# Performance work log

Measured on AMD Instinct MI355X. Metric: run time of the kernel, lower is better.

The kernel has to match this reference:

```python
import jax, jax.numpy as jnp
import numpy as np
import math

NP_, NA_ = 100000, 50000          # paper / author node counts
E0, E1, E2 = 300000, 300000, 200000  # author->paper, paper->author, paper->paper
H, D = 4, 16
HID = H * D                       # 64
IN_DIM, OUT_DIM = 128, 64
L = 2                             # num_layers
EPS = 1e-5


def _lin(x, W, b):
    return x @ W + b


def _ln(x, g, b):
    m = jnp.mean(x, axis=-1, keepdims=True)
    v = jnp.mean((x - m) ** 2, axis=-1, keepdims=True)
    return (x - m) * jax.lax.rsqrt(v + EPS) * g + b


def _segment_softmax(a, seg, n):
    m = jax.ops.segment_max(a, seg, num_segments=n)
    a = jnp.exp(a - m[seg])
    s = jax.ops.segment_sum(a, seg, num_segments=n)
    return a / (s[seg] + 1e-16)


def _hgt_conv(h_p, h_a, ei_ap, ei_pa, ei_pp,
              W_kqv, b_kqv, W_krel, W_vrel, p_rel, W_hout, b_hout, skip):
    # per-node-type fused KQV projection (HeteroDictLinear)
    kqv_p = _lin(h_p, W_kqv[0], b_kqv[0])   # [NP, 3*HID]
    kqv_a = _lin(h_a, W_kqv[1], b_kqv[1])   # [NA, 3*HID]
    k_p, q_p, v_p = [t.reshape(-1, H, D) for t in jnp.split(kqv_p, 3, axis=1)]
    k_a, q_a, v_a = [t.reshape(-1, H, D) for t in jnp.split(kqv_a, 3, axis=1)]
    # destination (query) concat order: paper then author -> dst offsets {paper:0, author:NP}
    Q = jnp.concatenate([q_p, q_a], axis=0)                    # [NP+NA, H, D]
    # per-(edge_type, head) DxD relation transforms on source k/v (k_rel / v_rel)
    # src concat order follows edge types: et0 src=author, et1 src=paper, et2 src=paper
    Ks = jnp.concatenate([
        jnp.einsum('nhd,hde->nhe', k_a, W_krel[0]),
        jnp.einsum('nhd,hde->nhe', k_p, W_krel[1]),
        jnp.einsum('nhd,hde->nhe', k_p, W_krel[2]),
    ], axis=0)                                                 # [NA+2*NP, H, D]
    Vs = jnp.concatenate([
        jnp.einsum('nhd,hde->nhe', v_a, W_vrel[0]),
        jnp.einsum('nhd,hde->nhe', v_p, W_vrel[1]),
        jnp.einsum('nhd,hde->nhe', v_p, W_vrel[2]),
    ], axis=0)
    # bipartite global edge index (src offsets: 0, NA, NA+NP; dst offsets: paper 0, author NP)
    src = jnp.concatenate([ei_ap[0], ei_pa[0] + NA_, ei_pp[0] + NA_ + NP_])
    dst = jnp.concatenate([ei_ap[1], ei_pa[1] + NP_, ei_pp[1]])
    p = jnp.concatenate([
        jnp.broadcast_to(p_rel[0], (E0, H)),
        jnp.broadcast_to(p_rel[1], (E1, H)),
        jnp.broadcast_to(p_rel[2], (E2, H)),
    ], axis=0)                                                 # [E, H]
    # edge-wise attention: alpha = (q_i * k_j).sum(-1) * p_rel / sqrt(D), segment-softmax over dst
    alpha = jnp.einsum('ehd,ehd->eh', Q[dst], Ks[src]) * p / math.sqrt(D)
    alpha = _segment_softmax(alpha, dst, NP_ + NA_)
    out = jax.ops.segment_sum(Vs[src] * alpha[:, :, None], dst,
                              num_segments=NP_ + NA_)          # [NP+NA, H, D]
    out = out.reshape(-1, HID)
    g = jax.nn.gelu(out, approximate=False)
    o_p = _lin(g[:NP_], W_hout[0], b_hout[0])
    o_a = _lin(g[NP_:], W_hout[1], b_hout[1])
    a_p = jax.nn.sigmoid(skip[0])
    a_a = jax.nn.sigmoid(skip[1])
    return a_p * o_p + (1.0 - a_p) * h_p, a_a * o_a + (1.0 - a_a) * h_a


def _forward(x_paper, x_author, ei_ap, ei_pa, ei_pp,
             W_in, b_in, W_kqv, b_kqv, W_krel, W_vrel, p_rel,
             W_hout, b_hout, skip, ln_g, ln_b, W_out, b_out):
    h_p = _lin(x_paper, W_in[0], b_in[0])
    h_a = _lin(x_author, W_in[1], b_in[1])
    for l in range(L):
        h_p, h_a = _hgt_conv(h_p, h_a, ei_ap, ei_pa, ei_pp,
                             W_kqv[l], b_kqv[l], W_krel[l], W_vrel[l],
                             p_rel[l], W_hout[l], b_hout[l], skip[l])
        h_p = jax.nn.gelu(_ln(h_p, ln_g[l, 0], ln_b[l, 0]), approximate=False)
        h_a = jax.nn.gelu(_ln(h_a, ln_g[l, 1], ln_b[l, 1]), approximate=False)
        # dropout is identity at eval
    out_p = _lin(h_p, W_out[0], b_out[0])
    out_a = _lin(h_a, W_out[1], b_out[1])
    return jnp.concatenate([out_p, out_a], axis=0)  # [NP+NA, OUT_DIM]


def setup_inputs() -> dict:
    key = jax.random.key(0)
    ks = jax.random.split(key, 20)
    f32 = jnp.float32

    def nrm(k, shape, fan_in):
        return jax.random.normal(k, shape, dtype=f32) * (1.0 / math.sqrt(fan_in))

    inp = {}
    inp['x_paper'] = jax.random.normal(ks[0], (NP_, IN_DIM), dtype=f32)
    inp['x_author'] = jax.random.normal(ks[1], (NA_, IN_DIM), dtype=f32)
    inp['ei_ap'] = jnp.stack([jax.random.randint(ks[2], (E0,), 0, NA_),
                              jax.random.randint(ks[3], (E0,), 0, NP_)]).astype(jnp.int32)
    inp['ei_pa'] = jnp.stack([jax.random.randint(ks[4], (E1,), 0, NP_),
                              jax.random.randint(ks[5], (E1,), 0, NA_)]).astype(jnp.int32)
    inp['ei_pp'] = jnp.stack([jax.random.randint(ks[6], (E2,), 0, NP_),
                              jax.random.randint(ks[7], (E2,), 0, NP_)]).astype(jnp.int32)
    inp['W_in'] = nrm(ks[8], (2, IN_DIM, HID), IN_DIM)
    inp['b_in'] = jnp.zeros((2, HID), f32)
    inp['W_kqv'] = nrm(ks[9], (L, 2, HID, 3 * HID), HID)
    inp['b_kqv'] = jnp.zeros((L, 2, 3 * HID), f32)
    inp['W_krel'] = nrm(ks[10], (L, 3, H, D, D), D)
    inp['W_vrel'] = nrm(ks[11], (L, 3, H, D, D), D)
    inp['p_rel'] = jnp.ones((L, 3, H), f32)
    inp['W_hout'] = nrm(ks[12], (L, 2, HID, HID), HID)
    inp['b_hout'] = jnp.zeros((L, 2, HID), f32)
    inp['skip'] = jnp.ones((L, 2), f32)
    inp['ln_g'] = jnp.ones((L, 2, HID), f32)
    inp['ln_b'] = jnp.zeros((L, 2, HID), f32)
    inp['W_out'] = nrm(ks[13], (2, HID, OUT_DIM), HID)
    inp['b_out'] = jnp.zeros((2, OUT_DIM), f32)
    return inp


def reference(x_paper, x_author, ei_ap, ei_pa, ei_pp,
              W_in, b_in, W_kqv, b_kqv, W_krel, W_vrel, p_rel,
              W_hout, b_hout, skip, ln_g, ln_b, W_out, b_out):
    return _forward(x_paper, x_author, ei_ap, ei_pa, ei_pp,
                    W_in, b_in, W_kqv, b_kqv, W_krel, W_vrel, p_rel,
                    W_hout, b_hout, skip, ln_g, ln_b, W_out, b_out)
```

## Files before the change

### kernel.cpp

```cpp
#include <hip/hip_runtime.h>
#include <hip/hip_bf16.h>

#define NP 100000
#define NA 50000
#define NTOT 150000
#define E0 300000
#define E1 300000
#define E2 200000
#define ETOT 800000
#define NH 4
#define HD 16
#define HID 64
#define IN_DIM 128
#define KQV 192
#define LAYERS 2
#define NSRC 250000
#define JP 320
#define JA 192
#define NCH 586
#define PT 1563
#define AT 782

typedef __attribute__((ext_vector_type(8))) short bf16x8;
typedef __attribute__((ext_vector_type(4))) float f32x4;
typedef _Float16 h16x2 __attribute__((ext_vector_type(2)));

__device__ __forceinline__ float gelu_exact(float x) {
    return 0.5f * x * (1.0f + erff(x * 0.7071067811865475f));
}
__device__ __forceinline__ unsigned short f2bf(float f) {
    unsigned u = __float_as_uint(f);
    return (unsigned short)((u + 0x7fffu + ((u >> 16) & 1u)) >> 16);
}
__device__ __forceinline__ float bf2f(unsigned short b) {
    return __uint_as_float((unsigned)b << 16);
}
__device__ __forceinline__ unsigned short f2h(float f) {
    union { _Float16 h; unsigned short u; } c;
    c.h = (_Float16)f;
    return c.u;
}

__device__ __forceinline__ void edge_decode(int e, const int* __restrict__ ei_ap,
                                            const int* __restrict__ ei_pa,
                                            const int* __restrict__ ei_pp,
                                            int& src, int& dst) {
    if (e < E0)            { src = ei_ap[e];                 dst = ei_ap[E0 + e]; }
    else if (e < E0 + E1)  { int le = e - E0;
                             src = NA + ei_pa[le];           dst = NP + ei_pa[E1 + le]; }
    else                   { int le = e - E0 - E1;
                             src = NA + NP + ei_pp[le];      dst = ei_pp[E2 + le]; }
}

__global__ void zero_int_kernel(int* __restrict__ p, int n) {
    int i = blockIdx.x * blockDim.x + threadIdx.x;
    int st = gridDim.x * blockDim.x;
    for (int j = i; j < n; j += st) p[j] = 0;
}

__global__ void csr_count_kernel(const int* __restrict__ ei_ap, const int* __restrict__ ei_pa,
                                 const int* __restrict__ ei_pp, int* __restrict__ cnt) {
    int e = blockIdx.x * 256 + threadIdx.x;
    if (e >= ETOT) return;
    int src, dst; edge_decode(e, ei_ap, ei_pa, ei_pp, src, dst);
    atomicAdd(&cnt[dst], 1);
}

__global__ void scan_chunk_sums(const int* __restrict__ cnt, int* __restrict__ csum) {
    __shared__ int sd[256];
    int c = blockIdx.x, t = threadIdx.x;
    int i = c * 256 + t;
    sd[t] = (i < NTOT) ? cnt[i] : 0;
    __syncthreads();
    for (int o = 128; o > 0; o >>= 1) { if (t < o) sd[t] += sd[t + o]; __syncthreads(); }
    if (t == 0) csum[c] = sd[0];
}

__global__ void scan_offsets(const int* __restrict__ csum, int* __restrict__ coff, int nch) {
    __shared__ int sd[1024];
    int t = threadIdx.x;
    int v = (t < nch) ? csum[t] : 0;
    sd[t] = v;
    __syncthreads();
    for (int o = 1; o < 1024; o <<= 1) {
        int x = (t >= o) ? sd[t - o] : 0;
        __syncthreads();
        sd[t] += x;
        __syncthreads();
    }
    if (t < nch) coff[t] = sd[t] - v;
}

__global__ void scan_final(const int* __restrict__ cnt, const int* __restrict__ coff,
                           int* __restrict__ row_ptr, int* __restrict__ cursor) {
    __shared__ int sd[256];
    int c = blockIdx.x, t = threadIdx.x, i = c * 256 + t;
    int v = (i < NTOT) ? cnt[i] : 0;
    sd[t] = v;
    __syncthreads();
    for (int o = 1; o < 256; o <<= 1) {
        int x = (t >= o) ? sd[t - o] : 0;
        __syncthreads();
        sd[t] += x;
        __syncthreads();
    }
    if (i < NTOT) { int ex = coff[c] + sd[t] - v; row_ptr[i] = ex; cursor[i] = ex; }
    if (i == 0) row_ptr[NTOT] = ETOT;
}

__global__ void csr_fill_kernel(const int* __restrict__ ei_ap, const int* __restrict__ ei_pa,
                                const int* __restrict__ ei_pp, int* __restrict__ cursor,
                                int* __restrict__ edge_src) {
    int e = blockIdx.x * 256 + threadIdx.x;
    if (e >= ETOT) return;
    int src, dst; edge_decode(e, ei_ap, ei_pa, ei_pp, src, dst);
    int pos = atomicAdd(&cursor[dst], 1);
    edge_src[pos] = src;
}

__global__ void prep_weights(const float* __restrict__ W_in, const float* __restrict__ W_hout,
                             const float* __restrict__ W_out,
                             unsigned short* __restrict__ WinT,
                             unsigned short* __restrict__ WhoutT,
                             unsigned short* __restrict__ WoutT) {
    int idx = blockIdx.x * 256 + threadIdx.x;
    if (idx < 2 * 64 * IN_DIM) {
        int t = idx >> 13, r = idx & 8191;
        int c = r >> 7, k = r & 127;
        WinT[idx] = f2bf(W_in[(size_t)t * IN_DIM * HID + (size_t)k * HID + c]);
        return;
    }
    int i2 = idx - 2 * 64 * IN_DIM;
    if (i2 < LAYERS * 2 * 4096) {
        int p = i2 >> 12, r = i2 & 4095;
        int c = r >> 6, k = r & 63;
        WhoutT[i2] = f2bf(W_hout[(size_t)p * 4096 + (size_t)k * HID + c]);
        return;
    }
    int i3 = i2 - LAYERS * 2 * 4096;
    if (i3 < 2 * 4096) {
        int p = i3 >> 12, r = i3 & 4095;
        int c = r >> 6, k = r & 63;
        WoutT[i3] = f2bf(W_out[(size_t)p * 4096 + (size_t)k * HID + c]);
    }
}

__global__ void fuse_weights_kernel(const float* __restrict__ Wkqv, const float* __restrict__ bkqv,
                                    const float* __restrict__ Wkrel, const float* __restrict__ Wvrel,
                                    unsigned short* __restrict__ WfpT, float* __restrict__ bfp,
                                    unsigned short* __restrict__ WfaT, float* __restrict__ bfa) {
    int idx = blockIdx.x * 256 + threadIdx.x;
    int type, i, j;
    if (idx < 65 * JP) { type = 0; i = idx / JP; j = idx % JP; }
    else {
        int r = idx - 65 * JP;
        if (r >= 65 * JA) return;
        type = 1; i = r / JA; j = r % JA;
    }
    int c = j >> 6, jj = j & 63, h = jj >> 4, e = jj & 15;
    const float* Wk = Wkqv + (size_t)type * HID * KQV;
    const float* bk = bkqv + type * KQV;
    float val;
    if (c == 0) {
        val = (i < 64) ? Wk[i * KQV + 64 + jj] : bk[64 + jj];
    } else {
        int et, isV;
        if (type == 0) { et = (c == 1 || c == 3) ? 1 : 2; isV = (c >= 3); }
        else           { et = 0; isV = (c == 2); }
        const float* Wr = (isV ? Wvrel : Wkrel) + (size_t)(et * NH + h) * HD * HD;
        int sb = (isV ? 128 : 0) + h * HD;
        val = 0.0f;
        #pragma unroll
        for (int d = 0; d < HD; d++) {
            float a = (i < 64) ? Wk[i * KQV + sb + d] : bk[sb + d];
            val += a * Wr[d * HD + e];
        }
    }
    if (i < 64) (type ? WfaT : WfpT)[(size_t)j * 64 + i] = f2bf(val);
    else        (type ? bfa : bfp)[j] = val;
}

__global__ __launch_bounds__(256) void gemm_in(
    const float* __restrict__ xp, const float* __restrict__ xa,
    const unsigned short* __restrict__ WinT, const float* __restrict__ b_in,
    unsigned short* __restrict__ Hb)
{
    __shared__ unsigned short Xb[64][136];
    __shared__ unsigned short Wt[64][136];
    int b = blockIdx.x, tid = threadIdx.x;
    int type = (b >= PT);
    int tile = type ? (b - PT) : b;
    int N = type ? NA : NP;
    const float* X = type ? xa : xp;
    const unsigned short* WT = WinT + (size_t)type * 64 * IN_DIM;
    const float* bias = b_in + type * HID;
    unsigned short* H = Hb + (type ? (size_t)NP * HID : 0);
    int nb = tile * 64;

    {
        int row = tid >> 2, c0 = (tid & 3) * 32;
        int n = nb + row;
        if (n < N) {
            const float* xr = X + (size_t)n * IN_DIM + c0;
            #pragma unroll
            for (int i = 0; i < 32; i += 4) {
                float4 v = *(const float4*)(xr + i);
                *(ushort4*)&Xb[row][c0 + i] =
                    make_ushort4(f2bf(v.x), f2bf(v.y), f2bf(v.z), f2bf(v.w));
            }
        } else {
            #pragma unroll
            for (int i = 0; i < 32; i += 4)
                *(ushort4*)&Xb[row][c0 + i] = make_ushort4(0, 0, 0, 0);
        }
    }
    #pragma unroll
    for (int it = 0; it < 8; it++) {
        int idx = it * 256 + tid;
        int c = idx >> 5, kg = (idx & 31) * 4;
        *(ushort4*)&Wt[c][kg] = *(const ushort4*)(WT + (size_t)c * IN_DIM + kg);
    }
    __syncthreads();

    int w = tid >> 6, lane = tid & 63;
    int wr = (w >> 1) * 32, wc = (w & 1) * 32;
    int lrow = lane & 15, lgrp = lane >> 4;

    f32x4 acc00 = {0.f, 0.f, 0.f, 0.f};
    f32x4 acc01 = {0.f, 0.f, 0.f, 0.f};
    f32x4 acc10 = {0.f, 0.f, 0.f, 0.f};
    f32x4 acc11 = {0.f, 0.f, 0.f, 0.f};
    #pragma unroll
    for (int ks = 0; ks < 4; ks++) {
        int ko = ks * 32 + lgrp * 8;
        bf16x8 a0 = *(const bf16x8*)&Xb[wr + lrow][ko];
        bf16x8 a1 = *(const bf16x8*)&Xb[wr + 16 + lrow][ko];
        bf16x8 b0 = *(const bf16x8*)&Wt[wc + lrow][ko];
        bf16x8 b1 = *(const bf16x8*)&Wt[wc + 16 + lrow][ko];
        acc00 = __builtin_amdgcn_mfma_f32_16x16x32_bf16(a0, b0, acc00, 0, 0, 0);
        acc01 = __builtin_amdgcn_mfma_f32_16x16x32_bf16(a0, b1, acc01, 0, 0, 0);
        acc10 = __builtin_amdgcn_mfma_f32_16x16x32_bf16(a1, b0, acc10, 0, 0, 0);
        acc11 = __builtin_amdgcn_mfma_f32_16x16x32_bf16(a1, b1, acc11, 0, 0, 0);
    }

    float bias0 = bias[wc + lrow], bias1 = bias[wc + 16 + lrow];
    int c0 = wc + lrow, c1 = wc + 16 + lrow;
    bool even = ((lrow & 1) == 0);
    #pragma unroll
    for (int mi = 0; mi < 2; mi++) {
        const f32x4 accn0 = mi ? acc10 : acc00;
        const f32x4 accn1 = mi ? acc11 : acc01;
        int rbase = wr + mi * 16 + lgrp * 4;
        #pragma unroll
        for (int r = 0; r < 4; r++) {
            int n = nb + rbase + r;
            unsigned own = (unsigned)f2bf(accn0[r] + bias0)
                         | ((unsigned)f2bf(accn1[r] + bias1) << 16);
            unsigned oth = __shfl_xor(own, 1, 64);
            if (even && n < N) {
                unsigned* hp = (unsigned*)(H + (size_t)n * HID);
                hp[c0 >> 1] = (own & 0xffffu) | (oth << 16);
                hp[c1 >> 1] = (own >> 16) | (oth & 0xffff0000u);
            }
        }
    }
}

__global__ __launch_bounds__(256) void gemm_kqv(
    const unsigned short* __restrict__ Hb,
    const unsigned short* __restrict__ WfpT, const float* __restrict__ bfp,
    const unsigned short* __restrict__ WfaT, const float* __restrict__ bfa,
    unsigned short* __restrict__ Qh, unsigned* __restrict__ KVb)
{
    __shared__ unsigned short Xb[64][72];
    __shared__ unsigned short WtQ[64][72];
    __shared__ unsigned short WtK[64][72];
    __shared__ unsigned short WtV[64][72];
    int b = blockIdx.x, tid = threadIdx.x;
    int type, tile;
    bool hasQ;
    int kcol, vcol, noff;
    if (b < PT)        { type = 0; tile = b;          hasQ = true;
                         kcol = 64;  vcol = 192; noff = NA; }
    else if (b < 2*PT) { type = 0; tile = b - PT;     hasQ = false;
                         kcol = 128; vcol = 256; noff = NA + NP; }
    else               { type = 1; tile = b - 2*PT;   hasQ = true;
                         kcol = 64;  vcol = 128; noff = 0; }
    int N = type ? NA : NP;
    const unsigned short* X = Hb + (type ? (size_t)NP * HID : 0);
    const unsigned short* WT = type ? WfaT : WfpT;
    const float* bias = type ? bfa : bfp;
    int nb = tile * 64;
    int qnoff = type ? NP : 0;

    {
        int row = tid >> 2, c0 = (tid & 3) * 16;
        int n = nb + row;
        if (n < N) {
            const unsigned short* xr = X + (size_t)n * HID + c0;
            *(ushort4*)&Xb[row][c0]      = *(const ushort4*)(xr);
            *(ushort4*)&Xb[row][c0 + 4]  = *(const ushort4*)(xr + 4);
            *(ushort4*)&Xb[row][c0 + 8]  = *(const ushort4*)(xr + 8);
            *(ushort4*)&Xb[row][c0 + 12] = *(const ushort4*)(xr + 12);
        } else {
            #pragma unroll
            for (int i = 0; i < 16; i += 4)
                *(ushort4*)&Xb[row][c0 + i] = make_ushort4(0, 0, 0, 0);
        }
    }
    #pragma unroll
    for (int it = 0; it < 4; it++) {
        int idx = it * 256 + tid;
        int c = idx >> 4, kg = (idx & 15) * 4;
        *(ushort4*)&WtK[c][kg] = *(const ushort4*)(WT + (size_t)(kcol + c) * 64 + kg);
        *(ushort4*)&WtV[c][kg] = *(const ushort4*)(WT + (size_t)(vcol + c) * 64 + kg);
        if (hasQ)
            *(ushort4*)&WtQ[c][kg] = *(const ushort4*)(WT + (size_t)c * 64 + kg);
    }
    __syncthreads();

    int w = tid >> 6, lane = tid & 63;
    int wr = (w >> 1) * 32, wc = (w & 1) * 32;
    int lrow = lane & 15, lgrp = lane >> 4;

    f32x4 q00 = {0.f,0.f,0.f,0.f}, q01 = {0.f,0.f,0.f,0.f};
    f32x4 q10 = {0.f,0.f,0.f,0.f}, q11 = {0.f,0.f,0.f,0.f};
    f32x4 k00 = {0.f,0.f,0.f,0.f}, k01 = {0.f,0.f,0.f,0.f};
    f32x4 k10 = {0.f,0.f,0.f,0.f}, k11 = {0.f,0.f,0.f,0.f};
    f32x4 v00 = {0.f,0.f,0.f,0.f}, v01 = {0.f,0.f,0.f,0.f};
    f32x4 v10 = {0.f,0.f,0.f,0.f}, v11 = {0.f,0.f,0.f,0.f};
    #pragma unroll
    for (int ks = 0; ks < 2; ks++) {
        int ko = ks * 32 + lgrp * 8;
        bf16x8 a0 = *(const bf16x8*)&Xb[wr + lrow][ko];
        bf16x8 a1 = *(const bf16x8*)&Xb[wr + 16 + lrow][ko];
        bf16x8 bk0 = *(const bf16x8*)&WtK[wc + lrow][ko];
        bf16x8 bk1 = *(const bf16x8*)&WtK[wc + 16 + lrow][ko];
        k00 = __builtin_amdgcn_mfma_f32_16x16x32_bf16(a0, bk0, k00, 0, 0, 0);
        k01 = __builtin_amdgcn_mfma_f32_16x16x32_bf16(a0, bk1, k01, 0, 0, 0);
        k10 = __builtin_amdgcn_mfma_f32_16x16x32_bf16(a1, bk0, k10, 0, 0, 0);
        k11 = __builtin_amdgcn_mfma_f32_16x16x32_bf16(a1, bk1, k11, 0, 0, 0);
        bf16x8 bv0 = *(const bf16x8*)&WtV[wc + lrow][ko];
        bf16x8 bv1 = *(const bf16x8*)&WtV[wc + 16 + lrow][ko];
        v00 = __builtin_amdgcn_mfma_f32_16x16x32_bf16(a0, bv0, v00, 0, 0, 0);
        v01 = __builtin_amdgcn_mfma_f32_16x16x32_bf16(a0, bv1, v01, 0, 0, 0);
        v10 = __builtin_amdgcn_mfma_f32_16x16x32_bf16(a1, bv0, v10, 0, 0, 0);
        v11 = __builtin_amdgcn_mfma_f32_16x16x32_bf16(a1, bv1, v11, 0, 0, 0);
        if (hasQ) {
            bf16x8 bq0 = *(const bf16x8*)&WtQ[wc + lrow][ko];
            bf16x8 bq1 = *(const bf16x8*)&WtQ[wc + 16 + lrow][ko];
            q00 = __builtin_amdgcn_mfma_f32_16x16x32_bf16(a0, bq0, q00, 0, 0, 0);
            q01 = __builtin_amdgcn_mfma_f32_16x16x32_bf16(a0, bq1, q01, 0, 0, 0);
            q10 = __builtin_amdgcn_mfma_f32_16x16x32_bf16(a1, bq0, q10, 0, 0, 0);
            q11 = __builtin_amdgcn_mfma_f32_16x16x32_bf16(a1, bq1, q11, 0, 0, 0);
        }
    }

    int c0 = wc + lrow, c1 = wc + 16 + lrow;
    bool even = ((lrow & 1) == 0);
    if (hasQ) {
        float bq0 = bias[c0], bq1 = bias[c1];
        #pragma unroll
        for (int mi = 0; mi < 2; mi++) {
            const f32x4 a0 = mi ? q10 : q00;
            const f32x4 a1 = mi ? q11 : q01;
            int rbase = wr + mi * 16 + lgrp * 4;
            #pragma unroll
            for (int r = 0; r < 4; r++) {
                int n = nb + rbase + r;
                unsigned own = (unsigned)f2h(a0[r] + bq0)
                             | ((unsigned)f2h(a1[r] + bq1) << 16);
                unsigned oth = __shfl_xor(own, 1, 64);
                if (even && n < N) {
                    unsigned* qp = (unsigned*)(Qh + (size_t)(qnoff + n) * HID);
                    qp[c0 >> 1] = (own & 0xffffu) | (oth << 16);
                    qp[c1 >> 1] = (own >> 16) | (oth & 0xffff0000u);
                }
            }
        }
    }
    {
        float bk0 = bias[kcol + c0], bk1 = bias[kcol + c1];
        float bv0 = bias[vcol + c0], bv1 = bias[vcol + c1];
        #pragma unroll
        for (int mi = 0; mi < 2; mi++) {
            const f32x4 ak0 = mi ? k10 : k00;
            const f32x4 ak1 = mi ? k11 : k01;
            const f32x4 av0 = mi ? v10 : v00;
            const f32x4 av1 = mi ? v11 : v01;
            int rbase = wr + mi * 16 + lgrp * 4;
            #pragma unroll
            for (int r = 0; r < 4; r++) {
                int n = nb + rbase + r;
                unsigned* dst = KVb + (((size_t)(noff + n)) << 6);
                unsigned own0 = (unsigned)f2h(ak0[r] + bk0) | ((unsigned)f2h(av0[r] + bv0) << 16);
                unsigned oth0 = __shfl_xor(own0, 1, 64);
                unsigned own1 = (unsigned)f2h(ak1[r] + bk1) | ((unsigned)f2h(av1[r] + bv1) << 16);
                unsigned oth1 = __shfl_xor(own1, 1, 64);
                if (n < N) {
                    unsigned w0 = even ? ((own0 & 0xffffu) | (oth0 << 16))
                                       : ((oth0 >> 16) | (own0 & 0xffff0000u));
                    unsigned w1 = even ? ((own1 & 0xffffu) | (oth1 << 16))
                                       : ((oth1 >> 16) | (own1 & 0xffff0000u));
                    dst[c0] = w0;
                    dst[c1] = w1;
                }
            }
        }
    }
}

__global__ __launch_bounds__(256) void attn_kernel(
    const unsigned short* __restrict__ Qh, const unsigned* __restrict__ KVb,
    const float* __restrict__ p_rel, const int* __restrict__ row_ptr,
    const int* __restrict__ edge_src, unsigned short* __restrict__ ABf)
{
    int wid = threadIdx.x >> 6, lane = threadIdx.x & 63;
    int n = blockIdx.x * 4 + wid;
    if (n >= NTOT) return;
    int half = lane >> 5;
    int p = lane & 31;
    int h = p >> 3;
    unsigned qw = *(const unsigned*)(Qh + (((size_t)n) << 6) + 2 * p);
    union { unsigned u; h16x2 v; _Float16 f[2]; } qc; qc.u = qw;
    h16x2 qh = qc.v;
    const float INV_LN2 = 1.4426950408889634f;
    float pr0 = p_rel[h] * 0.25f * INV_LN2;
    float pr1 = p_rel[4 + h] * 0.25f * INV_LN2;
    float pr2 = p_rel[8 + h] * 0.25f * INV_LN2;
    int beg = row_ptr[n], end = row_ptr[n + 1];
    float s = 0.0f, acc0 = 0.f, acc1 = 0.f;
    for (int e = beg; e < end; e += 4) {
        int e0 = e + half;
        int e1 = e + 2 + half;
        bool v0 = (e0 < end), v1 = (e1 < end);
        int s0 = v0 ? edge_src[e0] : 0;
        int s1 = v1 ? edge_src[e1] : 0;
        uint2 kv0 = *(const uint2*)(KVb + (((size_t)s0) << 6) + 2 * p);
        uint2 kv1 = *(const uint2*)(KVb + (((size_t)s1) << 6) + 2 * p);
        float d0, d1;
#if __has_builtin(__builtin_amdgcn_fdot2)
        {
            union { unsigned u; h16x2 v; } ck;
            ck.u = kv0.x; d0 = __builtin_amdgcn_fdot2(qh, ck.v, 0.0f, false);
            ck.u = kv1.x; d1 = __builtin_amdgcn_fdot2(qh, ck.v, 0.0f, false);
        }
#else
        {
            union { unsigned u; _Float16 f[2]; } ck;
            float q0 = (float)qc.f[0], q1 = (float)qc.f[1];
            ck.u = kv0.x; d0 = q0 * (float)ck.f[0] + q1 * (float)ck.f[1];
            ck.u = kv1.x; d1 = q0 * (float)ck.f[0] + q1 * (float)ck.f[1];
        }
#endif
        d0 += __shfl_xor(d0, 1, 64);  d1 += __shfl_xor(d1, 1, 64);
        d0 += __shfl_xor(d0, 2, 64);  d1 += __shfl_xor(d1, 2, 64);
        d0 += __shfl_xor(d0, 4, 64);  d1 += __shfl_xor(d1, 4, 64);
        float pa = (s0 < NA) ? pr0 : ((s0 < NA + NP) ? pr1 : pr2);
        float pb = (s1 < NA) ? pr0 : ((s1 < NA + NP) ? pr1 : pr2);
        float a0 = v0 ? fminf(d0 * pa, 80.0f) : -INFINITY;
        float a1 = v1 ? fminf(d1 * pb, 80.0f) : -INFINITY;
        float p0 = exp2f(a0);
        float p1 = exp2f(a1);
        s += p0 + p1;
        union { unsigned u; _Float16 f[2]; } cv0, cv1;
        cv0.u = kv0.y; cv1.u = kv1.y;
        acc0 += p0 * (float)cv0.f[0] + p1 * (float)cv1.f[0];
        acc1 += p0 * (float)cv0.f[1] + p1 * (float)cv1.f[1];
    }
    s    += __shfl_xor(s, 32, 64);
    acc0 += __shfl_xor(acc0, 32, 64);
    acc1 += __shfl_xor(acc1, 32, 64);
    if (half == 0) {
        float inv = 1.0f / (s + 1e-16f);
        unsigned pack = (unsigned)f2bf(acc0 * inv) | ((unsigned)f2bf(acc1 * inv) << 16);
        *(unsigned*)(ABf + (((size_t)n) << 6) + 2 * p) = pack;
    }
}

__global__ __launch_bounds__(256) void gemm_hout(
    const unsigned short* __restrict__ ABf, const unsigned short* __restrict__ WhT,
    const float* __restrict__ bhout, const float* __restrict__ skip_p,
    const float* __restrict__ lng, const float* __restrict__ lnb,
    unsigned short* __restrict__ Hb,
    const unsigned short* __restrict__ WoT, const float* __restrict__ bout,
    float* __restrict__ outp)
{
    __shared__ unsigned short Xb[64][72];
    __shared__ unsigned short Wt[64][72];
    __shared__ float hs[64][68];
    int b = blockIdx.x, tid = threadIdx.x;
    int type = (b >= PT);
    int tile = type ? (b - PT) : b;
    int N = type ? NA : NP;
    size_t base_off = type ? (size_t)NP * HID : 0;
    const unsigned short* X = ABf + base_off;
    const unsigned short* W = WhT + (size_t)type * 4096;
    const float* bias = bhout + type * HID;
    unsigned short* H = Hb + base_off;
    int nb = tile * 64;
    bool fuse_out = (WoT != nullptr);

    {
        int row = tid >> 2, c0 = (tid & 3) * 16;
        int n = nb + row;
        unsigned short tmp[16];
        if (n < N) {
            const unsigned short* xr = X + (((size_t)n) << 6) + c0;
            #pragma unroll
            for (int i = 0; i < 16; i += 4) {
                ushort4 v = *(const ushort4*)(xr + i);
                tmp[i]   = f2bf(gelu_exact(bf2f(v.x)));
                tmp[i+1] = f2bf(gelu_exact(bf2f(v.y)));
                tmp[i+2] = f2bf(gelu_exact(bf2f(v.z)));
                tmp[i+3] = f2bf(gelu_exact(bf2f(v.w)));
            }
        } else {
            #pragma unroll
            for (int i = 0; i < 16; i++) tmp[i] = 0;
        }
        #pragma unroll
        for (int i = 0; i < 16; i += 4)
            *(ushort4*)&Xb[row][c0 + i] = make_ushort4(tmp[i], tmp[i+1], tmp[i+2], tmp[i+3]);
    }
    #pragma unroll
    for (int it = 0; it < 4; it++) {
        int idx = it * 256 + tid;
        int c = idx >> 4, kg = (idx & 15) * 4;
        *(ushort4*)&Wt[c][kg] = *(const ushort4*)(W + (size_t)c * 64 + kg);
    }
    __syncthreads();

    int w = tid >> 6, lane = tid & 63;
    int wr = (w >> 1) * 32, wc = (w & 1) * 32;
    int lrow = lane & 15, lgrp = lane >> 4;

    f32x4 acc00 = {0.f, 0.f, 0.f, 0.f};
    f32x4 acc01 = {0.f, 0.f, 0.f, 0.f};
    f32x4 acc10 = {0.f, 0.f, 0.f, 0.f};
    f32x4 acc11 = {0.f, 0.f, 0.f, 0.f};
    #pragma unroll
    for (int ks = 0; ks < 2; ks++) {
        int ko = ks * 32 + lgrp * 8;
        bf16x8 a0 = *(const bf16x8*)&Xb[wr + lrow][ko];
        bf16x8 a1 = *(const bf16x8*)&Xb[wr + 16 + lrow][ko];
        bf16x8 b0 = *(const bf16x8*)&Wt[wc + lrow][ko];
        bf16x8 b1 = *(const bf16x8*)&Wt[wc + 16 + lrow][ko];
        acc00 = __builtin_amdgcn_mfma_f32_16x16x32_bf16(a0, b0, acc00, 0, 0, 0);
        acc01 = __builtin_amdgcn_mfma_f32_16x16x32_bf16(a0, b1, acc01, 0, 0, 0);
        acc10 = __builtin_amdgcn_mfma_f32_16x16x32_bf16(a1, b0, acc10, 0, 0, 0);
        acc11 = __builtin_amdgcn_mfma_f32_16x16x32_bf16(a1, b1, acc11, 0, 0, 0);
    }

    float a = 1.0f / (1.0f + __expf(-skip_p[type]));
    float oma = 1.0f - a;
    float bias0 = bias[wc + lrow], bias1 = bias[wc + 16 + lrow];
    #pragma unroll
    for (int mi = 0; mi < 2; mi++) {
        const f32x4 accn0 = mi ? acc10 : acc00;
        const f32x4 accn1 = mi ? acc11 : acc01;
        int rbase = wr + mi * 16 + lgrp * 4;
        #pragma unroll
        for (int r = 0; r < 4; r++) {
            int row = rbase + r;
            int n = nb + row;
            if (n < N) {
                const unsigned short* hp = H + (size_t)n * HID;
                hs[row][wc + lrow]      = a * (accn0[r] + bias0) + oma * bf2f(hp[wc + lrow]);
                hs[row][wc + 16 + lrow] = a * (accn1[r] + bias1) + oma * bf2f(hp[wc + 16 + lrow]);
            } else {
                hs[row][wc + lrow] = 0.f;
                hs[row][wc + 16 + lrow] = 0.f;
            }
        }
    }
    __syncthreads();

    const int tr = tid >> 4, tc = tid & 15;
    const int tcj = tc * 4;
    float g0 = lng[type*HID+tcj], g1 = lng[type*HID+tcj+1],
          g2 = lng[type*HID+tcj+2], g3 = lng[type*HID+tcj+3];
    float l0 = lnb[type*HID+tcj], l1 = lnb[type*HID+tcj+1],
          l2 = lnb[type*HID+tcj+2], l3 = lnb[type*HID+tcj+3];
    #pragma unroll 1
    for (int m = 0; m < 4; m++) {
        int row = tr * 4 + m;
        int n = nb + row;
        float v0 = hs[row][tcj], v1 = hs[row][tcj+1], v2 = hs[row][tcj+2], v3 = hs[row][tcj+3];
        float sum = v0 + v1 + v2 + v3;
        sum += __shfl_xor(sum, 1, 64); sum += __shfl_xor(sum, 2, 64);
        sum += __shfl_xor(sum, 4, 64); sum += __shfl_xor(sum, 8, 64);
        float mean = sum * (1.0f / 64.0f);
        float d0 = v0 - mean, d1 = v1 - mean, d2 = v2 - mean, d3 = v3 - mean;
        float sq = d0*d0 + d1*d1 + d2*d2 + d3*d3;
        sq += __shfl_xor(sq, 1, 64); sq += __shfl_xor(sq, 2, 64);
        sq += __shfl_xor(sq, 4, 64); sq += __shfl_xor(sq, 8, 64);
        float rstd = rsqrtf(sq * (1.0f / 64.0f) + 1e-5f);
        float r0 = gelu_exact(d0 * rstd * g0 + l0);
        float r1 = gelu_exact(d1 * rstd * g1 + l1);
        float r2 = gelu_exact(d2 * rstd * g2 + l2);
        float r3 = gelu_exact(d3 * rstd * g3 + l3);
        hs[row][tcj] = r0; hs[row][tcj+1] = r1;
        hs[row][tcj+2] = r2; hs[row][tcj+3] = r3;
        if (!fuse_out && n < N) {
            uint2 pk;
            pk.x = (unsigned)f2bf(r0) | ((unsigned)f2bf(r1) << 16);
            pk.y = (unsigned)f2bf(r2) | ((unsigned)f2bf(r3) << 16);
            *(uint2*)(H + (size_t)n * HID + tcj) = pk;
        }
    }

    if (fuse_out) {
        __syncthreads();
        {
            int row = tid >> 2, c0 = (tid & 3) * 16;
            #pragma unroll
            for (int i = 0; i < 16; i += 4) {
                *(ushort4*)&Xb[row][c0 + i] = make_ushort4(
                    f2bf(hs[row][c0 + i]),     f2bf(hs[row][c0 + i + 1]),
                    f2bf(hs[row][c0 + i + 2]), f2bf(hs[row][c0 + i + 3]));
            }
        }
        const unsigned short* W2 = WoT + (size_t)type * 4096;
        #pragma unroll
        for (int it = 0; it < 4; it++) {
            int idx = it * 256 + tid;
            int c = idx >> 4, kg = (idx & 15) * 4;
            *(ushort4*)&Wt[c][kg] = *(const ushort4*)(W2 + (size_t)c * 64 + kg);
        }
        __syncthreads();

        f32x4 o00 = {0.f,0.f,0.f,0.f}, o01 = {0.f,0.f,0.f,0.f};
        f32x4 o10 = {0.f,0.f,0.f,0.f}, o11 = {0.f,0.f,0.f,0.f};
        #pragma unroll
        for (int ks = 0; ks < 2; ks++) {
            int ko = ks * 32 + lgrp * 8;
            bf16x8 a0 = *(const bf16x8*)&Xb[wr + lrow][ko];
            bf16x8 a1 = *(const bf16x8*)&Xb[wr + 16 + lrow][ko];
            bf16x8 b0 = *(const bf16x8*)&Wt[wc + lrow][ko];
            bf16x8 b1 = *(const bf16x8*)&Wt[wc + 16 + lrow][ko];
            o00 = __builtin_amdgcn_mfma_f32_16x16x32_bf16(a0, b0, o00, 0, 0, 0);
            o01 = __builtin_amdgcn_mfma_f32_16x16x32_bf16(a0, b1, o01, 0, 0, 0);
            o10 = __builtin_amdgcn_mfma_f32_16x16x32_bf16(a1, b0, o10, 0, 0, 0);
            o11 = __builtin_amdgcn_mfma_f32_16x16x32_bf16(a1, b1, o11, 0, 0, 0);
        }
        const float* b2 = bout + type * HID;
        float b20 = b2[wc + lrow], b21 = b2[wc + 16 + lrow];
        float* O = outp + base_off;
        #pragma unroll
        for (int mi = 0; mi < 2; mi++) {
            const f32x4 on0 = mi ? o10 : o00;
            const f32x4 on1 = mi ? o11 : o01;
            int rbase = wr + mi * 16 + lgrp * 4;
            #pragma unroll
            for (int r = 0; r < 4; r++) {
                int n = nb + rbase + r;
                if (n >= N) continue;
                O[(size_t)n * HID + wc + lrow]      = on0[r] + b20;
                O[(size_t)n * HID + wc + 16 + lrow] = on1[r] + b21;
            }
        }
    }
}

extern "C" void kernel_launch(void* const* d_in, const int* in_sizes, int n_in,
                              void* d_out, int out_size, void* d_ws, size_t ws_size,
                              hipStream_t stream) {
    const float* x_paper  = (const float*)d_in[0];
    const float* x_author = (const float*)d_in[1];
    const int*   ei_ap    = (const int*)d_in[2];
    const int*   ei_pa    = (const int*)d_in[3];
    const int*   ei_pp    = (const int*)d_in[4];
    const float* W_in     = (const float*)d_in[5];
    const float* b_in     = (const float*)d_in[6];
    const float* W_kqv    = (const float*)d_in[7];
    const float* b_kqv    = (const float*)d_in[8];
    const float* W_krel   = (const float*)d_in[9];
    const float* W_vrel   = (const float*)d_in[10];
    const float* p_rel    = (const float*)d_in[11];
    const float* W_hout   = (const float*)d_in[12];
    const float* b_hout   = (const float*)d_in[13];
    const float* skip     = (const float*)d_in[14];
    const float* ln_g     = (const float*)d_in[15];
    const float* ln_b     = (const float*)d_in[16];
    const float* W_out    = (const float*)d_in[17];
    const float* b_out    = (const float*)d_in[18];
    float* out            = (float*)d_out;

    char* ws = (char*)d_ws;
    unsigned short* Hb  = (unsigned short*)ws;
    unsigned short* Qh  = Hb + (size_t)NTOT * HID;
    unsigned* KVb       = (unsigned*)(Qh + (size_t)NTOT * HID);
    unsigned short* ABf = (unsigned short*)(KVb + (size_t)NSRC * HID);
    unsigned short* WfpT = ABf + (size_t)NTOT * HID;
    float* bfp  = (float*)(WfpT + (size_t)JP * 64);
    unsigned short* WfaT = (unsigned short*)(bfp + JP);
    float* bfa  = (float*)(WfaT + (size_t)JA * 64);
    unsigned short* WinT   = (unsigned short*)(bfa + JA);
    unsigned short* WhoutT = WinT + 2 * 64 * IN_DIM;
    unsigned short* WoutT  = WhoutT + LAYERS * 2 * 64 * 64;
    int* cnt      = (int*)(WoutT + 2 * 64 * 64);
    int* row_ptr  = cnt + NTOT;
    int* cursor   = row_ptr + NTOT + 16;
    int* edge_src = cursor + NTOT;
    int* csum     = edge_src + ETOT;
    int* coff     = csum + 1024;

    dim3 blk(256);
    const int EB = (ETOT + 255) / 256;

    zero_int_kernel<<<256, blk, 0, stream>>>(cnt, NTOT);
    csr_count_kernel<<<EB, blk, 0, stream>>>(ei_ap, ei_pa, ei_pp, cnt);
    scan_chunk_sums<<<NCH, blk, 0, stream>>>(cnt, csum);
    scan_offsets<<<1, 1024, 0, stream>>>(csum, coff, NCH);
    scan_final<<<NCH, blk, 0, stream>>>(cnt, coff, row_ptr, cursor);
    csr_fill_kernel<<<EB, blk, 0, stream>>>(ei_ap, ei_pa, ei_pp, cursor, edge_src);

    prep_weights<<<(2*64*IN_DIM + LAYERS*2*4096 + 2*4096 + 255) / 256, blk, 0, stream>>>(
        W_in, W_hout, W_out, WinT, WhoutT, WoutT);

    gemm_in<<<PT + AT, blk, 0, stream>>>(x_paper, x_author, WinT, b_in, Hb);

    for (int l = 0; l < LAYERS; l++) {
        fuse_weights_kernel<<<(65 * JP + 65 * JA + 255) / 256, blk, 0, stream>>>(
            W_kqv + (size_t)l * 2 * HID * KQV, b_kqv + (size_t)l * 2 * KQV,
            W_krel + (size_t)l * 3 * NH * HD * HD, W_vrel + (size_t)l * 3 * NH * HD * HD,
            WfpT, bfp, WfaT, bfa);
        gemm_kqv<<<2 * PT + AT, blk, 0, stream>>>(
            Hb, WfpT, bfp, WfaT, bfa, Qh, KVb);
        attn_kernel<<<(NTOT + 3) / 4, blk, 0, stream>>>(
            Qh, KVb, p_rel + l * 3 * NH, row_ptr, edge_src, ABf);
        bool last = (l == LAYERS - 1);
        gemm_hout<<<PT + AT, blk, 0, stream>>>(
            ABf, WhoutT + (size_t)l * 2 * 4096, b_hout + l * 2 * HID,
            skip + l * 2, ln_g + l * 2 * HID, ln_b + l * 2 * HID, Hb,
            last ? WoutT : nullptr, last ? b_out : nullptr, last ? out : nullptr);
    }
}
```

Measured before the change: 365.4 us.

## Fuse KQV projection into input and output GEMM epilogues, batch weight fusion

The separate gemm_kqv kernel is removed. The KQV projection now runs inside the input-projection kernel and inside the previous layer's hout/LayerNorm kernel, reading the freshly computed hidden tile from shared memory instead of reloading H from global memory. Fused weights for both layers are precomputed in one launch, and the zero kernel is replaced by hipMemsetAsync. This cuts kernel launches and one global read of H per layer, at the cost of more shared memory, more barriers and longer per-block work in the fused kernels.

```diff
diff --git a/kernel.cpp b/kernel.cpp
--- a/kernel.cpp
+++ b/kernel.cpp
@@ -20,6 +20,7 @@
 #define NCH 586
 #define PT 1563
 #define AT 782
+#define LSPAN 33280
 
 typedef __attribute__((ext_vector_type(8))) short bf16x8;
 typedef __attribute__((ext_vector_type(4))) float f32x4;
@@ -50,12 +51,6 @@
                              src = NA + ei_pa[le];           dst = NP + ei_pa[E1 + le]; }
     else                   { int le = e - E0 - E1;
                              src = NA + NP + ei_pp[le];      dst = ei_pp[E2 + le]; }
-}
-
-__global__ void zero_int_kernel(int* __restrict__ p, int n) {
-    int i = blockIdx.x * blockDim.x + threadIdx.x;
-    int st = gridDim.x * blockDim.x;
-    for (int j = i; j < n; j += st) p[j] = 0;
 }
 
 __global__ void csr_count_kernel(const int* __restrict__ ei_ap, const int* __restrict__ ei_pa,
@@ -145,21 +140,32 @@
     }
 }
 
-__global__ void fuse_weights_kernel(const float* __restrict__ Wkqv, const float* __restrict__ bkqv,
-                                    const float* __restrict__ Wkrel, const float* __restrict__ Wvrel,
-                                    unsigned short* __restrict__ WfpT, float* __restrict__ bfp,
-                                    unsigned short* __restrict__ WfaT, float* __restrict__ bfa) {
-    int idx = blockIdx.x * 256 + threadIdx.x;
+__global__ void fuse_weights_all(const float* __restrict__ Wkqv, const float* __restrict__ bkqv,
+                                 const float* __restrict__ Wkrel, const float* __restrict__ Wvrel,
+                                 unsigned short* __restrict__ WfpT, float* __restrict__ bfp,
+                                 unsigned short* __restrict__ WfaT, float* __restrict__ bfa) {
+    int gidx = blockIdx.x * 256 + threadIdx.x;
+    if (gidx >= LAYERS * LSPAN) return;
+    int lay = gidx / LSPAN;
+    int idx = gidx - lay * LSPAN;
+    const float* Wkqv_l = Wkqv + (size_t)lay * 2 * HID * KQV;
+    const float* bkqv_l = bkqv + (size_t)lay * 2 * KQV;
+    const float* Wkrel_l = Wkrel + (size_t)lay * 3 * NH * HD * HD;
+    const float* Wvrel_l = Wvrel + (size_t)lay * 3 * NH * HD * HD;
+    unsigned short* WfpT_l = WfpT + (size_t)lay * JP * 64;
+    unsigned short* WfaT_l = WfaT + (size_t)lay * JA * 64;
+    float* bfp_l = bfp + (size_t)lay * JP;
+    float* bfa_l = bfa + (size_t)lay * JA;
+
     int type, i, j;
     if (idx < 65 * JP) { type = 0; i = idx / JP; j = idx % JP; }
     else {
         int r = idx - 65 * JP;
-        if (r >= 65 * JA) return;
         type = 1; i = r / JA; j = r % JA;
     }
     int c = j >> 6, jj = j & 63, h = jj >> 4, e = jj & 15;
-    const float* Wk = Wkqv + (size_t)type * HID * KQV;
-    const float* bk = bkqv + type * KQV;
+    const float* Wk = Wkqv_l + (size_t)type * HID * KQV;
+    const float* bk = bkqv_l + type * KQV;
     float val;
     if (c == 0) {
         val = (i < 64) ? Wk[i * KQV + 64 + jj] : bk[64 + jj];
@@ -167,7 +173,7 @@
         int et, isV;
         if (type == 0) { et = (c == 1 || c == 3) ? 1 : 2; isV = (c >= 3); }
         else           { et = 0; isV = (c == 2); }
-        const float* Wr = (isV ? Wvrel : Wkrel) + (size_t)(et * NH + h) * HD * HD;
+        const float* Wr = (isV ? Wvrel_l : Wkrel_l) + (size_t)(et * NH + h) * HD * HD;
         int sb = (isV ? 128 : 0) + h * HD;
         val = 0.0f;
         #pragma unroll
@@ -176,17 +182,143 @@
             val += a * Wr[d * HD + e];
         }
     }
-    if (i < 64) (type ? WfaT : WfpT)[(size_t)j * 64 + i] = f2bf(val);
-    else        (type ? bfa : bfp)[j] = val;
-}
-
-__global__ __launch_bounds__(256) void gemm_in(
+    if (i < 64) (type ? WfaT_l : WfpT_l)[(size_t)j * 64 + i] = f2bf(val);
+    else        (type ? bfa_l : bfp_l)[j] = val;
+}
+
+__device__ __forceinline__ void mfma64(const unsigned short* A, const unsigned short* W,
+                                       int wr, int wc, int lrow, int lgrp,
+                                       f32x4& a00, f32x4& a01, f32x4& a10, f32x4& a11) {
+    a00 = (f32x4){0.f,0.f,0.f,0.f}; a01 = a00; a10 = a00; a11 = a00;
+    #pragma unroll
+    for (int ks = 0; ks < 2; ks++) {
+        int ko = ks * 32 + lgrp * 8;
+        bf16x8 x0 = *(const bf16x8*)&A[(wr + lrow) * 72 + ko];
+        bf16x8 x1 = *(const bf16x8*)&A[(wr + 16 + lrow) * 72 + ko];
+        bf16x8 w0 = *(const bf16x8*)&W[(wc + lrow) * 72 + ko];
+        bf16x8 w1 = *(const bf16x8*)&W[(wc + 16 + lrow) * 72 + ko];
+        a00 = __builtin_amdgcn_mfma_f32_16x16x32_bf16(x0, w0, a00, 0, 0, 0);
+        a01 = __builtin_amdgcn_mfma_f32_16x16x32_bf16(x0, w1, a01, 0, 0, 0);
+        a10 = __builtin_amdgcn_mfma_f32_16x16x32_bf16(x1, w0, a10, 0, 0, 0);
+        a11 = __builtin_amdgcn_mfma_f32_16x16x32_bf16(x1, w1, a11, 0, 0, 0);
+    }
+}
+
+__device__ __forceinline__ void store_q(f32x4 a00, f32x4 a01, f32x4 a10, f32x4 a11,
+                                        float bq0, float bq1, int c0, int c1, bool even,
+                                        int nb, int N, int wr, int lgrp,
+                                        unsigned short* Qbase) {
+    #pragma unroll
+    for (int mi = 0; mi < 2; mi++) {
+        const f32x4 a0 = mi ? a10 : a00;
+        const f32x4 a1 = mi ? a11 : a01;
+        int rbase = wr + mi * 16 + lgrp * 4;
+        #pragma unroll
+        for (int r = 0; r < 4; r++) {
+            int n = nb + rbase + r;
+            unsigned own = (unsigned)f2h(a0[r] + bq0) | ((unsigned)f2h(a1[r] + bq1) << 16);
+            unsigned oth = __shfl_xor(own, 1, 64);
+            if (even && n < N) {
+                unsigned* qp = (unsigned*)(Qbase + (size_t)n * HID);
+                qp[c0 >> 1] = (own & 0xffffu) | (oth << 16);
+                qp[c1 >> 1] = (own >> 16) | (oth & 0xffff0000u);
+            }
+        }
+    }
+}
+
+__device__ __forceinline__ void store_kv(f32x4 k00, f32x4 k01, f32x4 k10, f32x4 k11,
+                                         f32x4 v00, f32x4 v01, f32x4 v10, f32x4 v11,
+                                         float bk0, float bk1, float bv0, float bv1,
+                                         int c0, int c1, bool even,
+                                         int nb, int N, int wr, int lgrp,
+                                         int noff, unsigned* KVb) {
+    #pragma unroll
+    for (int mi = 0; mi < 2; mi++) {
+        const f32x4 ak0 = mi ? k10 : k00;
+        const f32x4 ak1 = mi ? k11 : k01;
+        const f32x4 av0 = mi ? v10 : v00;
+        const f32x4 av1 = mi ? v11 : v01;
+        int rbase = wr + mi * 16 + lgrp * 4;
+        #pragma unroll
+        for (int r = 0; r < 4; r++) {
+            int n = nb + rbase + r;
+            unsigned own0 = (unsigned)f2h(ak0[r] + bk0) | ((unsigned)f2h(av0[r] + bv0) << 16);
+            unsigned oth0 = __shfl_xor(own0, 1, 64);
+            unsigned own1 = (unsigned)f2h(ak1[r] + bk1) | ((unsigned)f2h(av1[r] + bv1) << 16);
+            unsigned oth1 = __shfl_xor(own1, 1, 64);
+            if (n < N) {
+                unsigned* dst = KVb + (((size_t)(noff + n)) << 6);
+                unsigned w0 = even ? ((own0 & 0xffffu) | (oth0 << 16))
+                                   : ((oth0 >> 16) | (own0 & 0xffff0000u));
+                unsigned w1 = even ? ((own1 & 0xffffu) | (oth1 << 16))
+                                   : ((oth1 >> 16) | (own1 & 0xffff0000u));
+                dst[c0] = w0;
+                dst[c1] = w1;
+            }
+        }
+    }
+}
+
+__device__ __forceinline__ void kqv_phase(const unsigned short* HS,
+                                          unsigned short* PA, unsigned short* PB,
+                                          const unsigned short* WT, const float* bias2,
+                                          int type, int tid, int nb, int N,
+                                          int wr, int wc, int lrow, int lgrp,
+                                          int c0, int c1, bool even,
+                                          unsigned short* Qh, unsigned* KVb) {
+    #pragma unroll
+    for (int it = 0; it < 4; it++) {
+        int idx = it * 256 + tid;
+        int c = idx >> 4, kg = (idx & 15) * 4;
+        *(ushort4*)&PA[c * 72 + kg] = *(const ushort4*)(WT + (size_t)c * 64 + kg);
+    }
+    __syncthreads();
+    {
+        f32x4 q00, q01, q10, q11;
+        mfma64(HS, PA, wr, wc, lrow, lgrp, q00, q01, q10, q11);
+        store_q(q00, q01, q10, q11, bias2[c0], bias2[c1], c0, c1, even,
+                nb, N, wr, lgrp, Qh + (size_t)(type ? NP : 0) * HID);
+    }
+    __syncthreads();
+    int ng = type ? 1 : 2;
+    for (int g = 0; g < ng; g++) {
+        int kc = type ? 64 : (g ? 128 : 64);
+        int vc = type ? 128 : (g ? 256 : 192);
+        int nf = type ? 0 : (g ? NA + NP : NA);
+        #pragma unroll
+        for (int it = 0; it < 4; it++) {
+            int idx = it * 256 + tid;
+            int c = idx >> 4, kg = (idx & 15) * 4;
+            *(ushort4*)&PA[c * 72 + kg] = *(const ushort4*)(WT + (size_t)(kc + c) * 64 + kg);
+            *(ushort4*)&PB[c * 72 + kg] = *(const ushort4*)(WT + (size_t)(vc + c) * 64 + kg);
+        }
+        __syncthreads();
+        f32x4 k00, k01, k10, k11, v00, v01, v10, v11;
+        mfma64(HS, PA, wr, wc, lrow, lgrp, k00, k01, k10, k11);
+        mfma64(HS, PB, wr, wc, lrow, lgrp, v00, v01, v10, v11);
+        store_kv(k00, k01, k10, k11, v00, v01, v10, v11,
+                 bias2[kc + c0], bias2[kc + c1], bias2[vc + c0], bias2[vc + c1],
+                 c0, c1, even, nb, N, wr, lgrp, nf, KVb);
+        __syncthreads();
+    }
+}
+
+__global__ __launch_bounds__(256) void gemm_in_kqv(
     const float* __restrict__ xp, const float* __restrict__ xa,
     const unsigned short* __restrict__ WinT, const float* __restrict__ b_in,
-    unsigned short* __restrict__ Hb)
+    const unsigned short* __restrict__ WfpT, const float* __restrict__ bfp,
+    const unsigned short* __restrict__ WfaT, const float* __restrict__ bfa,
+    unsigned short* __restrict__ Hb, unsigned short* __restrict__ Qh,
+    unsigned* __restrict__ KVb)
 {
-    __shared__ unsigned short Xb[64][136];
-    __shared__ unsigned short Wt[64][136];
+    __shared__ unsigned short smem[17408];
+    unsigned short* XB  = smem;
+    unsigned short* WTl = smem + 8704;
+    unsigned short* HS  = smem;
+    unsigned short* PA  = smem + 4608;
+    unsigned short* PB  = smem + 9216;
+
     int b = blockIdx.x, tid = threadIdx.x;
     int type = (b >= PT);
     int tile = type ? (b - PT) : b;
@@ -198,54 +330,53 @@
     int nb = tile * 64;
 
     {
-        int row = tid >> 2, c0 = (tid & 3) * 32;
+        int row = tid >> 2, cg = (tid & 3) * 32;
         int n = nb + row;
         if (n < N) {
-            const float* xr = X + (size_t)n * IN_DIM + c0;
+            const float* xr = X + (size_t)n * IN_DIM + cg;
             #pragma unroll
             for (int i = 0; i < 32; i += 4) {
                 float4 v = *(const float4*)(xr + i);
-                *(ushort4*)&Xb[row][c0 + i] =
+                *(ushort4*)&XB[row * 136 + cg + i] =
                     make_ushort4(f2bf(v.x), f2bf(v.y), f2bf(v.z), f2bf(v.w));
             }
         } else {
             #pragma unroll
             for (int i = 0; i < 32; i += 4)
-                *(ushort4*)&Xb[row][c0 + i] = make_ushort4(0, 0, 0, 0);
+                *(ushort4*)&XB[row * 136 + cg + i] = make_ushort4(0, 0, 0, 0);
         }
     }
     #pragma unroll
     for (int it = 0; it < 8; it++) {
         int idx = it * 256 + tid;
         int c = idx >> 5, kg = (idx & 31) * 4;
-        *(ushort4*)&Wt[c][kg] = *(const ushort4*)(WT + (size_t)c * IN_DIM + kg);
+        *(ushort4*)&WTl[c * 136 + kg] = *(const ushort4*)(WT + (size_t)c * IN_DIM + kg);
     }
     __syncthreads();
 
     int w = tid >> 6, lane = tid & 63;
     int wr = (w >> 1) * 32, wc = (w & 1) * 32;
     int lrow = lane & 15, lgrp = lane >> 4;
-
-    f32x4 acc00 = {0.f, 0.f, 0.f, 0.f};
-    f32x4 acc01 = {0.f, 0.f, 0.f, 0.f};
-    f32x4 acc10 = {0.f, 0.f, 0.f, 0.f};
-    f32x4 acc11 = {0.f, 0.f, 0.f, 0.f};
+    int c0 = wc + lrow, c1 = wc + 16 + lrow;
+    bool even = ((lrow & 1) == 0);
+
+    f32x4 acc00 = {0.f,0.f,0.f,0.f}, acc01 = {0.f,0.f,0.f,0.f};
+    f32x4 acc10 = {0.f,0.f,0.f,0.f}, acc11 = {0.f,0.f,0.f,0.f};
     #pragma unroll
     for (int ks = 0; ks < 4; ks++) {
         int ko = ks * 32 + lgrp * 8;
-        bf16x8 a0 = *(const bf16x8*)&Xb[wr + lrow][ko];
-        bf16x8 a1 = *(const bf16x8*)&Xb[wr + 16 + lrow][ko];
-        bf16x8 b0 = *(const bf16x8*)&Wt[wc + lrow][ko];
-        bf16x8 b1 = *(const bf16x8*)&Wt[wc + 16 + lrow][ko];
+        bf16x8 a0 = *(const bf16x8*)&XB[(wr + lrow) * 136 + ko];
+        bf16x8 a1 = *(const bf16x8*)&XB[(wr + 16 + lrow) * 136 + ko];
+        bf16x8 b0 = *(const bf16x8*)&WTl[(wc + lrow) * 136 + ko];
+        bf16x8 b1 = *(const bf16x8*)&WTl[(wc + 16 + lrow) * 136 + ko];
         acc00 = __builtin_amdgcn_mfma_f32_16x16x32_bf16(a0, b0, acc00, 0, 0, 0);
         acc01 = __builtin_amdgcn_mfma_f32_16x16x32_bf16(a0, b1, acc01, 0, 0, 0);
         acc10 = __builtin_amdgcn_mfma_f32_16x16x32_bf16(a1, b0, acc10, 0, 0, 0);
         acc11 = __builtin_amdgcn_mfma_f32_16x16x32_bf16(a1, b1, acc11, 0, 0, 0);
     }
-
-    float bias0 = bias[wc + lrow], bias1 = bias[wc + 16 + lrow];
-    int c0 = wc + lrow, c1 = wc + 16 + lrow;
-    bool even = ((lrow & 1) == 0);
+    __syncthreads();
+
+    float bias0 = bias[c0], bias1 = bias[c1];
     #pragma unroll
     for (int mi = 0; mi < 2; mi++) {
         const f32x4 accn0 = mi ? acc10 : acc00;
@@ -254,8 +385,11 @@
         #pragma unroll
         for (int r = 0; r < 4; r++) {
             int n = nb + rbase + r;
-            unsigned own = (unsigned)f2bf(accn0[r] + bias0)
-                         | ((unsigned)f2bf(accn1[r] + bias1) << 16);
+            unsigned short h0 = f2bf(accn0[r] + bias0);
+            unsigned short h1 = f2bf(accn1[r] + bias1);
+            HS[(rbase + r) * 72 + c0] = h0;
+            HS[(rbase + r) * 72 + c1] = h1;
+            unsigned own = (unsigned)h0 | ((unsigned)h1 << 16);
             unsigned oth = __shfl_xor(own, 1, 64);
             if (even && n < N) {
                 unsigned* hp = (unsigned*)(H + (size_t)n * HID);
@@ -264,150 +398,12 @@
             }
         }
     }
-}
-
-__global__ __launch_bounds__(256) void gemm_kqv(
-    const unsigned short* __restrict__ Hb,
-    const unsigned short* __restrict__ WfpT, const float* __restrict__ bfp,
-    const unsigned short* __restrict__ WfaT, const float* __restrict__ bfa,
-    unsigned short* __restrict__ Qh, unsigned* __restrict__ KVb)
-{
-    __shared__ unsigned short Xb[64][72];
-    __shared__ unsigned short WtQ[64][72];
-    __shared__ unsigned short WtK[64][72];
-    __shared__ unsigned short WtV[64][72];
-    int b = blockIdx.x, tid = threadIdx.x;
-    int type, tile;
-    bool hasQ;
-    int kcol, vcol, noff;
-    if (b < PT)        { type = 0; tile = b;          hasQ = true;
-                         kcol = 64;  vcol = 192; noff = NA; }
-    else if (b < 2*PT) { type = 0; tile = b - PT;     hasQ = false;
-                         kcol = 128; vcol = 256; noff = NA + NP; }
-    else               { type = 1; tile = b - 2*PT;   hasQ = true;
-                         kcol = 64;  vcol = 128; noff = 0; }
-    int N = type ? NA : NP;
-    const unsigned short* X = Hb + (type ? (size_t)NP * HID : 0);
-    const unsigned short* WT = type ? WfaT : WfpT;
-    const float* bias = type ? bfa : bfp;
-    int nb = tile * 64;
-    int qnoff = type ? NP : 0;
-
-    {
-        int row = tid >> 2, c0 = (tid & 3) * 16;
-        int n = nb + row;
-        if (n < N) {
-            const unsigned short* xr = X + (size_t)n * HID + c0;
-            *(ushort4*)&Xb[row][c0]      = *(const ushort4*)(xr);
-            *(ushort4*)&Xb[row][c0 + 4]  = *(const ushort4*)(xr + 4);
-            *(ushort4*)&Xb[row][c0 + 8]  = *(const ushort4*)(xr + 8);
-            *(ushort4*)&Xb[row][c0 + 12] = *(const ushort4*)(xr + 12);
-        } else {
-            #pragma unroll
-            for (int i = 0; i < 16; i += 4)
-                *(ushort4*)&Xb[row][c0 + i] = make_ushort4(0, 0, 0, 0);
-        }
-    }
-    #pragma unroll
-    for (int it = 0; it < 4; it++) {
-        int idx = it * 256 + tid;
-        int c = idx >> 4, kg = (idx & 15) * 4;
-        *(ushort4*)&WtK[c][kg] = *(const ushort4*)(WT + (size_t)(kcol + c) * 64 + kg);
-        *(ushort4*)&WtV[c][kg] = *(const ushort4*)(WT + (size_t)(vcol + c) * 64 + kg);
-        if (hasQ)
-            *(ushort4*)&WtQ[c][kg] = *(const ushort4*)(WT + (size_t)c * 64 + kg);
-    }
-    __syncthreads();
-
-    int w = tid >> 6, lane = tid & 63;
-    int wr = (w >> 1) * 32, wc = (w & 1) * 32;
-    int lrow = lane & 15, lgrp = lane >> 4;
-
-    f32x4 q00 = {0.f,0.f,0.f,0.f}, q01 = {0.f,0.f,0.f,0.f};
-    f32x4 q10 = {0.f,0.f,0.f,0.f}, q11 = {0.f,0.f,0.f,0.f};
-    f32x4 k00 = {0.f,0.f,0.f,0.f}, k01 = {0.f,0.f,0.f,0.f};
-    f32x4 k10 = {0.f,0.f,0.f,0.f}, k11 = {0.f,0.f,0.f,0.f};
-    f32x4 v00 = {0.f,0.f,0.f,0.f}, v01 = {0.f,0.f,0.f,0.f};
-    f32x4 v10 = {0.f,0.f,0.f,0.f}, v11 = {0.f,0.f,0.f,0.f};
-    #pragma unroll
-    for (int ks = 0; ks < 2; ks++) {
-        int ko = ks * 32 + lgrp * 8;
-        bf16x8 a0 = *(const bf16x8*)&Xb[wr + lrow][ko];
-        bf16x8 a1 = *(const bf16x8*)&Xb[wr + 16 + lrow][ko];
-        bf16x8 bk0 = *(const bf16x8*)&WtK[wc + lrow][ko];
-        bf16x8 bk1 = *(const bf16x8*)&WtK[wc + 16 + lrow][ko];
-        k00 = __builtin_amdgcn_mfma_f32_16x16x32_bf16(a0, bk0, k00, 0, 0, 0);
-        k01 = __builtin_amdgcn_mfma_f32_16x16x32_bf16(a0, bk1, k01, 0, 0, 0);
-        k10 = __builtin_amdgcn_mfma_f32_16x16x32_bf16(a1, bk0, k10, 0, 0, 0);
-        k11 = __builtin_amdgcn_mfma_f32_16x16x32_bf16(a1, bk1, k11, 0, 0, 0);
-        bf16x8 bv0 = *(const bf16x8*)&WtV[wc + lrow][ko];
-        bf16x8 bv1 = *(const bf16x8*)&WtV[wc + 16 + lrow][ko];
-        v00 = __builtin_amdgcn_mfma_f32_16x16x32_bf16(a0, bv0, v00, 0, 0, 0);
-        v01 = __builtin_amdgcn_mfma_f32_16x16x32_bf16(a0, bv1, v01, 0, 0, 0);
-        v10 = __builtin_amdgcn_mfma_f32_16x16x32_bf16(a1, bv0, v10, 0, 0, 0);
-        v11 = __builtin_amdgcn_mfma_f32_16x16x32_bf16(a1, bv1, v11, 0, 0, 0);
-        if (hasQ) {
-            bf16x8 bq0 = *(const bf16x8*)&WtQ[wc + lrow][ko];
-            bf16x8 bq1 = *(const bf16x8*)&WtQ[wc + 16 + lrow][ko];
-            q00 = __builtin_amdgcn_mfma_f32_16x16x32_bf16(a0, bq0, q00, 0, 0, 0);
-            q01 = __builtin_amdgcn_mfma_f32_16x16x32_bf16(a0, bq1, q01, 0, 0, 0);
-            q10 = __builtin_amdgcn_mfma_f32_16x16x32_bf16(a1, bq0, q10, 0, 0, 0);
-            q11 = __builtin_amdgcn_mfma_f32_16x16x32_bf16(a1, bq1, q11, 0, 0, 0);
-        }
-    }
-
-    int c0 = wc + lrow, c1 = wc + 16 + lrow;
-    bool even = ((lrow & 1) == 0);
-    if (hasQ) {
-        float bq0 = bias[c0], bq1 = bias[c1];
-        #pragma unroll
-        for (int mi = 0; mi < 2; mi++) {
-            const f32x4 a0 = mi ? q10 : q00;
-            const f32x4 a1 = mi ? q11 : q01;
-            int rbase = wr + mi * 16 + lgrp * 4;
-            #pragma unroll
-            for (int r = 0; r < 4; r++) {
-                int n = nb + rbase + r;
-                unsigned own = (unsigned)f2h(a0[r] + bq0)
-                             | ((unsigned)f2h(a1[r] + bq1) << 16);
-                unsigned oth = __shfl_xor(own, 1, 64);
-                if (even && n < N) {
-                    unsigned* qp = (unsigned*)(Qh + (size_t)(qnoff + n) * HID);
-                    qp[c0 >> 1] = (own & 0xffffu) | (oth << 16);
-                    qp[c1 >> 1] = (own >> 16) | (oth & 0xffff0000u);
-                }
-            }
-        }
-    }
-    {
-        float bk0 = bias[kcol + c0], bk1 = bias[kcol + c1];
-        float bv0 = bias[vcol + c0], bv1 = bias[vcol + c1];
-        #pragma unroll
-        for (int mi = 0; mi < 2; mi++) {
-            const f32x4 ak0 = mi ? k10 : k00;
-            const f32x4 ak1 = mi ? k11 : k01;
-            const f32x4 av0 = mi ? v10 : v00;
-            const f32x4 av1 = mi ? v11 : v01;
-            int rbase = wr + mi * 16 + lgrp * 4;
-            #pragma unroll
-            for (int r = 0; r < 4; r++) {
-                int n = nb + rbase + r;
-                unsigned* dst = KVb + (((size_t)(noff + n)) << 6);
-                unsigned own0 = (unsigned)f2h(ak0[r] + bk0) | ((unsigned)f2h(av0[r] + bv0) << 16);
-                unsigned oth0 = __shfl_xor(own0, 1, 64);
-                unsigned own1 = (unsigned)f2h(ak1[r] + bk1) | ((unsigned)f2h(av1[r] + bv1) << 16);
-                unsigned oth1 = __shfl_xor(own1, 1, 64);
-                if (n < N) {
-                    unsigned w0 = even ? ((own0 & 0xffffu) | (oth0 << 16))
-                                       : ((oth0 >> 16) | (own0 & 0xffff0000u));
-                    unsigned w1 = even ? ((own1 & 0xffffu) | (oth1 << 16))
-                                       : ((oth1 >> 16) | (own1 & 0xffff0000u));
-                    dst[c0] = w0;
-                    dst[c1] = w1;
-                }
-            }
-        }
-    }
+    __syncthreads();
+
+    const unsigned short* WT2 = type ? WfaT : WfpT;
+    const float* bias2 = type ? bfa : bfp;
+    kqv_phase(HS, PA, PB, WT2, bias2, type, tid, nb, N,
+              wr, wc, lrow, lgrp, c0, c1, even, Qh, KVb);
 }
 
 __global__ __launch_bounds__(256) void attn_kernel(
@@ -478,16 +474,20 @@
     }
 }
 
-__global__ __launch_bounds__(256) void gemm_hout(
+__global__ __launch_bounds__(256) void gemm_hout_fused(
     const unsigned short* __restrict__ ABf, const unsigned short* __restrict__ WhT,
     const float* __restrict__ bhout, const float* __restrict__ skip_p,
     const float* __restrict__ lng, const float* __restrict__ lnb,
     unsigned short* __restrict__ Hb,
+    const unsigned short* __restrict__ WfpT, const float* __restrict__ bfp,
+    const unsigned short* __restrict__ WfaT, const float* __restrict__ bfa,
+    unsigned short* __restrict__ Qh, unsigned* __restrict__ KVb,
     const unsigned short* __restrict__ WoT, const float* __restrict__ bout,
     float* __restrict__ outp)
 {
-    __shared__ unsigned short Xb[64][72];
-    __shared__ unsigned short Wt[64][72];
+    __shared__ unsigned short XbS[64 * 72];
+    __shared__ unsigned short PA[64 * 72];
+    __shared__ unsigned short PB[64 * 72];
     __shared__ float hs[64][68];
     int b = blockIdx.x, tid = threadIdx.x;
     int type = (b >= PT);
@@ -499,14 +499,14 @@
     const float* bias = bhout + type * HID;
     unsigned short* H = Hb + base_off;
     int nb = tile * 64;
-    bool fuse_out = (WoT != nullptr);
+    bool fin = (WoT != nullptr);
 
     {
-        int row = tid >> 2, c0 = (tid & 3) * 16;
+        int row = tid >> 2, cg = (tid & 3) * 16;
         int n = nb + row;
         unsigned short tmp[16];
         if (n < N) {
-            const unsigned short* xr = X + (((size_t)n) << 6) + c0;
+            const unsigned short* xr = X + (((size_t)n) << 6) + cg;
             #pragma unroll
             for (int i = 0; i < 16; i += 4) {
                 ushort4 v = *(const ushort4*)(xr + i);
@@ -521,40 +521,29 @@
         }
         #pragma unroll
         for (int i = 0; i < 16; i += 4)
-            *(ushort4*)&Xb[row][c0 + i] = make_ushort4(tmp[i], tmp[i+1], tmp[i+2], tmp[i+3]);
+            *(ushort4*)&XbS[row * 72 + cg + i] =
+                make_ushort4(tmp[i], tmp[i+1], tmp[i+2], tmp[i+3]);
     }
     #pragma unroll
     for (int it = 0; it < 4; it++) {
         int idx = it * 256 + tid;
         int c = idx >> 4, kg = (idx & 15) * 4;
-        *(ushort4*)&Wt[c][kg] = *(const ushort4*)(W + (size_t)c * 64 + kg);
+        *(ushort4*)&PA[c * 72 + kg] = *(const ushort4*)(W + (size_t)c * 64 + kg);
     }
     __syncthreads();
 
     int w = tid >> 6, lane = tid & 63;
     int wr = (w >> 1) * 32, wc = (w & 1) * 32;
     int lrow = lane & 15, lgrp = lane >> 4;
-
-    f32x4 acc00 = {0.f, 0.f, 0.f, 0.f};
-    f32x4 acc01 = {0.f, 0.f, 0.f, 0.f};
-    f32x4 acc10 = {0.f, 0.f, 0.f, 0.f};
-    f32x4 acc11 = {0.f, 0.f, 0.f, 0.f};
-    #pragma unroll
-    for (int ks = 0; ks < 2; ks++) {
-        int ko = ks * 32 + lgrp * 8;
-        bf16x8 a0 = *(const bf16x8*)&Xb[wr + lrow][ko];
-        bf16x8 a1 = *(const bf16x8*)&Xb[wr + 16 + lrow][ko];
-        bf16x8 b0 = *(const bf16x8*)&Wt[wc + lrow][ko];
-        bf16x8 b1 = *(const bf16x8*)&Wt[wc + 16 + lrow][ko];
-        acc00 = __builtin_amdgcn_mfma_f32_16x16x32_bf16(a0, b0, acc00, 0, 0, 0);
-        acc01 = __builtin_amdgcn_mfma_f32_16x16x32_bf16(a0, b1, acc01, 0, 0, 0);
-        acc10 = __builtin_amdgcn_mfma_f32_16x16x32_bf16(a1, b0, acc10, 0, 0, 0);
-        acc11 = __builtin_amdgcn_mfma_f32_16x16x32_bf16(a1, b1, acc11, 0, 0, 0);
-    }
+    int c0 = wc + lrow, c1 = wc + 16 + lrow;
+    bool even = ((lrow & 1) == 0);
+
+    f32x4 acc00, acc01, acc10, acc11;
+    mfma64(XbS, PA, wr, wc, lrow, lgrp, acc00, acc01, acc10, acc11);
 
     float a = 1.0f / (1.0f + __expf(-skip_p[type]));
     float oma = 1.0f - a;
-    float bias0 = bias[wc + lrow], bias1 = bias[wc + 16 + lrow];
+    float bias0 = bias[c0], bias1 = bias[c1];
     #pragma unroll
     for (int mi = 0; mi < 2; mi++) {
         const f32x4 accn0 = mi ? acc10 : acc00;
@@ -566,11 +555,11 @@
             int n = nb + row;
             if (n < N) {
                 const unsigned short* hp = H + (size_t)n * HID;
-                hs[row][wc + lrow]      = a * (accn0[r] + bias0) + oma * bf2f(hp[wc + lrow]);
-                hs[row][wc + 16 + lrow] = a * (accn1[r] + bias1) + oma * bf2f(hp[wc + 16 + lrow]);
+                hs[row][c0] = a * (accn0[r] + bias0) + oma * bf2f(hp[c0]);
+                hs[row][c1] = a * (accn1[r] + bias1) + oma * bf2f(hp[c1]);
             } else {
-                hs[row][wc + lrow] = 0.f;
-                hs[row][wc + 16 + lrow] = 0.f;
+                hs[row][c0] = 0.f;
+                hs[row][c1] = 0.f;
             }
         }
     }
@@ -602,50 +591,38 @@
         float r3 = gelu_exact(d3 * rstd * g3 + l3);
         hs[row][tcj] = r0; hs[row][tcj+1] = r1;
         hs[row][tcj+2] = r2; hs[row][tcj+3] = r3;
-        if (!fuse_out && n < N) {
+        if (!fin && n < N) {
             uint2 pk;
             pk.x = (unsigned)f2bf(r0) | ((unsigned)f2bf(r1) << 16);
             pk.y = (unsigned)f2bf(r2) | ((unsigned)f2bf(r3) << 16);
             *(uint2*)(H + (size_t)n * HID + tcj) = pk;
         }
     }
-
-    if (fuse_out) {
-        __syncthreads();
-        {
-            int row = tid >> 2, c0 = (tid & 3) * 16;
-            #pragma unroll
-            for (int i = 0; i < 16; i += 4) {
-                *(ushort4*)&Xb[row][c0 + i] = make_ushort4(
-                    f2bf(hs[row][c0 + i]),     f2bf(hs[row][c0 + i + 1]),
-                    f2bf(hs[row][c0 + i + 2]), f2bf(hs[row][c0 + i + 3]));
-            }
-        }
+    __syncthreads();
+
+    {
+        int row = tid >> 2, cg = (tid & 3) * 16;
+        #pragma unroll
+        for (int i = 0; i < 16; i += 4) {
+            *(ushort4*)&XbS[row * 72 + cg + i] = make_ushort4(
+                f2bf(hs[row][cg + i]),     f2bf(hs[row][cg + i + 1]),
+                f2bf(hs[row][cg + i + 2]), f2bf(hs[row][cg + i + 3]));
+        }
+    }
+
+    if (fin) {
         const unsigned short* W2 = WoT + (size_t)type * 4096;
         #pragma unroll
         for (int it = 0; it < 4; it++) {
             int idx = it * 256 + tid;
             int c = idx >> 4, kg = (idx & 15) * 4;
-            *(ushort4*)&Wt[c][kg] = *(const ushort4*)(W2 + (size_t)c * 64 + kg);
+            *(ushort4*)&PA[c * 72 + kg] = *(const ushort4*)(W2 + (size_t)c * 64 + kg);
         }
         __syncthreads();
-
-        f32x4 o00 = {0.f,0.f,0.f,0.f}, o01 = {0.f,0.f,0.f,0.f};
-        f32x4 o10 = {0.f,0.f,0.f,0.f}, o11 = {0.f,0.f,0.f,0.f};
-        #pragma unroll
-        for (int ks = 0; ks < 2; ks++) {
-            int ko = ks * 32 + lgrp * 8;
-            bf16x8 a0 = *(const bf16x8*)&Xb[wr + lrow][ko];
-            bf16x8 a1 = *(const bf16x8*)&Xb[wr + 16 + lrow][ko];
-            bf16x8 b0 = *(const bf16x8*)&Wt[wc + lrow][ko];
-            bf16x8 b1 = *(const bf16x8*)&Wt[wc + 16 + lrow][ko];
-            o00 = __builtin_amdgcn_mfma_f32_16x16x32_bf16(a0, b0, o00, 0, 0, 0);
-            o01 = __builtin_amdgcn_mfma_f32_16x16x32_bf16(a0, b1, o01, 0, 0, 0);
-            o10 = __builtin_amdgcn_mfma_f32_16x16x32_bf16(a1, b0, o10, 0, 0, 0);
-            o11 = __builtin_amdgcn_mfma_f32_16x16x32_bf16(a1, b1, o11, 0, 0, 0);
-        }
+        f32x4 o00, o01, o10, o11;
+        mfma64(XbS, PA, wr, wc, lrow, lgrp, o00, o01, o10, o11);
         const float* b2 = bout + type * HID;
-        float b20 = b2[wc + lrow], b21 = b2[wc + 16 + lrow];
+        float b20 = b2[c0], b21 = b2[c1];
         float* O = outp + base_off;
         #pragma unroll
         for (int mi = 0; mi < 2; mi++) {
@@ -656,10 +633,16 @@
             for (int r = 0; r < 4; r++) {
                 int n = nb + rbase + r;
                 if (n >= N) continue;
-                O[(size_t)n * HID + wc + lrow]      = on0[r] + b20;
-                O[(size_t)n * HID + wc + 16 + lrow] = on1[r] + b21;
+                O[(size_t)n * HID + c0] = on0[r] + b20;
+                O[(size_t)n * HID + c1] = on1[r] + b21;
             }
         }
+    } else {
+        __syncthreads();
+        const unsigned short* WT2 = type ? WfaT : WfpT;
+        const float* bias2 = type ? bfa : bfp;
+        kqv_phase(XbS, PA, PB, WT2, bias2, type, tid, nb, N,
+                  wr, wc, lrow, lgrp, c0, c1, even, Qh, KVb);
     }
 }
 
@@ -693,10 +676,10 @@
     unsigned* KVb       = (unsigned*)(Qh + (size_t)NTOT * HID);
     unsigned short* ABf = (unsigned short*)(KVb + (size_t)NSRC * HID);
     unsigned short* WfpT = ABf + (size_t)NTOT * HID;
-    float* bfp  = (float*)(WfpT + (size_t)JP * 64);
-    unsigned short* WfaT = (unsigned short*)(bfp + JP);
-    float* bfa  = (float*)(WfaT + (size_t)JA * 64);
-    unsigned short* WinT   = (unsigned short*)(bfa + JA);
+    float* bfp  = (float*)(WfpT + (size_t)2 * JP * 64);
+    unsigned short* WfaT = (unsigned short*)(bfp + 2 * JP);
+    float* bfa  = (float*)(WfaT + (size_t)2 * JA * 64);
+    unsigned short* WinT   = (unsigned short*)(bfa + 2 * JA);
     unsigned short* WhoutT = WinT + 2 * 64 * IN_DIM;
     unsigned short* WoutT  = WhoutT + LAYERS * 2 * 64 * 64;
     int* cnt      = (int*)(WoutT + 2 * 64 * 64);
@@ -709,7 +692,7 @@
     dim3 blk(256);
     const int EB = (ETOT + 255) / 256;
 
-    zero_int_kernel<<<256, blk, 0, stream>>>(cnt, NTOT);
+    hipMemsetAsync(cnt, 0, NTOT * sizeof(int), stream);
     csr_count_kernel<<<EB, blk, 0, stream>>>(ei_ap, ei_pa, ei_pp, cnt);
     scan_chunk_sums<<<NCH, blk, 0, stream>>>(cnt, csum);
     scan_offsets<<<1, 1024, 0, stream>>>(csum, coff, NCH);
@@ -718,22 +701,23 @@
 
     prep_weights<<<(2*64*IN_DIM + LAYERS*2*4096 + 2*4096 + 255) / 256, blk, 0, stream>>>(
         W_in, W_hout, W_out, WinT, WhoutT, WoutT);
-
-    gemm_in<<<PT + AT, blk, 0, stream>>>(x_paper, x_author, WinT, b_in, Hb);
-
-    for (int l = 0; l < LAYERS; l++) {
-        fuse_weights_kernel<<<(65 * JP + 65 * JA + 255) / 256, blk, 0, stream>>>(
-            W_kqv + (size_t)l * 2 * HID * KQV, b_kqv + (size_t)l * 2 * KQV,
-            W_krel + (size_t)l * 3 * NH * HD * HD, W_vrel + (size_t)l * 3 * NH * HD * HD,
-            WfpT, bfp, WfaT, bfa);
-        gemm_kqv<<<2 * PT + AT, blk, 0, stream>>>(
-            Hb, WfpT, bfp, WfaT, bfa, Qh, KVb);
-        attn_kernel<<<(NTOT + 3) / 4, blk, 0, stream>>>(
-            Qh, KVb, p_rel + l * 3 * NH, row_ptr, edge_src, ABf);
-        bool last = (l == LAYERS - 1);
-        gemm_hout<<<PT + AT, blk, 0, stream>>>(
-            ABf, WhoutT + (size_t)l * 2 * 4096, b_hout + l * 2 * HID,
-            skip + l * 2, ln_g + l * 2 * HID, ln_b + l * 2 * HID, Hb,
-            last ? WoutT : nullptr, last ? b_out : nullptr, last ? out : nullptr);
-    }
-}
+    fuse_weights_all<<<(LAYERS * LSPAN + 255) / 256, blk, 0, stream>>>(
+        W_kqv, b_kqv, W_krel, W_vrel, WfpT, bfp, WfaT, bfa);
+
+    gemm_in_kqv<<<PT + AT, blk, 0, stream>>>(
+        x_paper, x_author, WinT, b_in,
+        WfpT, bfp, WfaT, bfa, Hb, Qh, KVb);
+    attn_kernel<<<(NTOT + 3) / 4, blk, 0, stream>>>(
+        Qh, KVb, p_rel, row_ptr, edge_src, ABf);
+    gemm_hout_fused<<<PT + AT, blk, 0, stream>>>(
+        ABf, WhoutT, b_hout, skip, ln_g, ln_b, Hb,
+        WfpT + (size_t)JP * 64, bfp + JP, WfaT + (size_t)JA * 64, bfa + JA,
+        Qh, KVb, nullptr, nullptr, nullptr);
+    attn_kernel<<<(NTOT + 3) / 4, blk, 0, stream>>>(
+        Qh, KVb, p_rel + 3 * NH, row_ptr, edge_src, ABf);
+    gemm_hout_fused<<<PT + AT, blk, 0, stream>>>(
+        ABf, WhoutT + (size_t)2 * 4096, b_hout + 2 * HID, skip + 2,
+        ln_g + 2 * HID, ln_b + 2 * HID, Hb,
+        nullptr, nullptr, nullptr, nullptr, Qh, KVb,
+        WoutT, b_out, out);
+}
```

Result: no change. 364.1 us (-0.3%).
